# Optimization experiments

Measured on AMD Instinct MI355X. Metric: run time of the kernel, lower is better.

The kernel has to match this reference:

```python
import jax, jax.numpy as jnp
import numpy as np

N_POINTS = 1048576
N_LEVELS = 16
F = 2
BASE_RES = 16
FINEST_RES = 512
LOG2_HASH = 19
SIZES = [2 ** min(i + 1, LOG2_HASH) for i in range(N_LEVELS)]  # per-level table rows (powers of 2)
OFFS = np.concatenate([[0], np.cumsum(SIZES)]).astype(np.int64)  # static row offsets into packed table
TOTAL_ROWS = int(OFFS[-1])  # 131070
# hash primes from the torch module; uint32 wraparound matches int64 low-bit behavior
# because each table size is a power of two <= 2^19 < 2^32, so h % 2^k == low k bits.
P0, P1, P2, P3 = np.uint32(1), np.uint32(2654435761), np.uint32(29675113), np.uint32(123456789)
CORNERS = np.array([[0,0,0],[1,0,0],[0,1,0],[1,1,0],
                    [0,0,1],[1,0,1],[0,1,1],[1,1,1]], dtype=np.uint32)  # torch stacking order


def setup_inputs() -> dict:
    key = jax.random.key(0)
    k1, k2 = jax.random.split(key)
    coords = jax.random.uniform(k1, (N_POINTS, 3), dtype=jnp.float32, minval=-1.0, maxval=1.0)
    hash_init_scale = 0.001
    table = jax.random.uniform(k2, (TOTAL_ROWS, F), dtype=jnp.float32,
                               minval=-hash_init_scale, maxval=hash_init_scale)
    return {"coords": coords, "table": table}


def _encode(coords, table):
    corners = jnp.asarray(CORNERS)  # [8,3] uint32
    outs = []
    for level in range(N_LEVELS):
        res = min(BASE_RES * (2 ** level), FINEST_RES)
        cs = (coords + 1.0) * res           # [N,3]
        cf = jnp.floor(cs)
        frac = cs - cf                      # [N,3]
        base = cf.astype(jnp.uint32)        # coords >= -1 so floor >= 0
        c = base[None, :, :] + corners[:, None, :]   # [8,N,3]
        x, y, z = c[..., 0], c[..., 1], c[..., 2]
        h = x * P0
        h = h * P1 + y
        h = h * P2 + z
        h = h * P3
        h = (h & jnp.uint32(SIZES[level] - 1)).astype(jnp.int32)  # mod power-of-2 table size
        feats = table[int(OFFS[level]) + h]          # [8,N,F] gather
        tx = frac[..., 0:1]; ty = frac[..., 1:2]; tz = frac[..., 2:3]
        f = (feats[0] * (1 - tx) * (1 - ty) * (1 - tz)
             + feats[1] * tx * (1 - ty) * (1 - tz)
             + feats[2] * (1 - tx) * ty * (1 - tz)
             + feats[3] * tx * ty * (1 - tz)
             + feats[4] * (1 - tx) * (1 - ty) * tz
             + feats[5] * tx * (1 - ty) * tz
             + feats[6] * (1 - tx) * ty * tz
             + feats[7] * tx * ty * tz)              # [N,F]
        outs.append(f)
    return jnp.concatenate(outs, axis=-1)            # [N, N_LEVELS*F]


def reference(coords, table):
    return _encode(coords, table)
```

## Files before the change

### kernel.cpp

```cpp
#include <hip/hip_runtime.h>
#include <hip/hip_fp16.h>


#define BLOCK 1024
#define NBLOCKS 512
#define ITERS 16
#define STAGED_ROWS 32766
#define LDS_BYTES 131072

__device__ __forceinline__ float2 ldsRow(const unsigned* lds, unsigned idx) {
    unsigned u = lds[idx];
    __half2 h = *(__half2*)&u;
    return __half22float2(h);
}

#define PREP(FRES, HARR, WARR) \
    unsigned HARR[8]; float WARR[8]; { \
        const float csx = (px + 1.0f) * (FRES); \
        const float csy = (py + 1.0f) * (FRES); \
        const float csz = (pz + 1.0f) * (FRES); \
        const float cfx = floorf(csx), cfy = floorf(csy), cfz = floorf(csz); \
        const float tx = csx - cfx, ty = csy - cfy, tz = csz - cfz; \
        const unsigned hh = (unsigned)cfx * HA + (unsigned)cfy * HB + (unsigned)cfz * HC; \
        const float ux = 1.0f - tx, uy = 1.0f - ty, uz = 1.0f - tz; \
        WARR[0] = ux*uy*uz; WARR[1] = tx*uy*uz; WARR[2] = ux*ty*uz; WARR[3] = tx*ty*uz; \
        WARR[4] = ux*uy*tz; WARR[5] = tx*uy*tz; WARR[6] = ux*ty*tz; WARR[7] = tx*ty*tz; \
        HARR[0] = hh;           HARR[1] = hh + HA;           \
        HARR[2] = hh + HB;      HARR[3] = hh + HA + HB;      \
        HARR[4] = hh + HC;      HARR[5] = hh + HA + HC;      \
        HARR[6] = hh + HB + HC; HARR[7] = hh + HA + HB + HC; \
    }

#define GATHER_LDS(HARR, WARR, MASK, OFF, O0, O1) \
    { _Pragma("unroll") for (int c = 0; c < 8; ++c) { \
        float2 f = ldsRow(lds_tb, (OFF) + ((HARR[c]) & (MASK))); \
        (O0) += f.x * WARR[c]; (O1) += f.y * WARR[c]; } }

#define GATHER_GBL(HARR, WARR, MASK, OFF, O0, O1) \
    { _Pragma("unroll") for (int c = 0; c < 8; ++c) { \
        float2 f = tb[(OFF) + ((HARR[c]) & (MASK))]; \
        (O0) += f.x * WARR[c]; (O1) += f.y * WARR[c]; } }

__global__ __launch_bounds__(BLOCK) void ngp_encode_kernel(
    const float* __restrict__ coords,
    const float* __restrict__ table,
    float* __restrict__ out)
{
    extern __shared__ unsigned lds_tb[];

    {
        const float4* __restrict__ t4 = (const float4*)table;
        uint2* __restrict__ l2 = (uint2*)lds_tb;
        for (int r = threadIdx.x; r < STAGED_ROWS / 2; r += BLOCK) {
            float4 v = t4[r];
            __half2 a = __floats2half2_rn(v.x, v.y);
            __half2 b = __floats2half2_rn(v.z, v.w);
            uint2 u;
            u.x = *(unsigned*)&a;
            u.y = *(unsigned*)&b;
            l2[r] = u;
        }
    }
    __syncthreads();

    constexpr unsigned P1 = 2654435761u, P2 = 29675113u, P3 = 123456789u;
    constexpr unsigned HA = P1 * P2 * P3;
    constexpr unsigned HB = P2 * P3;
    constexpr unsigned HC = P3;

    const float2* __restrict__ tb = (const float2*)table;
    float4* __restrict__ out4 = (float4*)out;

    const int q = threadIdx.x & 7;
    const int l0 = 2 * q;
    const unsigned mask0 = (2u << l0) - 1u, off0 = mask0 - 1u;
    const unsigned mask1 = (4u << l0) - 1u, off1 = mask1 - 1u;
    const float fres0 = (l0 < 5) ? (float)(16 << l0) : 512.0f;
    const float fres1 = (l0 < 4) ? (float)(32 << l0) : 512.0f;

    for (int it = 0; it < ITERS; ++it) {
        const int t = (blockIdx.x * ITERS + it) * BLOCK + threadIdx.x;
        const int p = t >> 3;

        const float px = coords[3 * p + 0];
        const float py = coords[3 * p + 1];
        const float pz = coords[3 * p + 2];

        PREP(fres0, h0, w0)
        PREP(fres1, h1, w1)

        float o0 = 0.0f, o1 = 0.0f, o2 = 0.0f, o3 = 0.0f;
        if (q != 7) {
            GATHER_LDS(h0, w0, mask0, off0, o0, o1)
            GATHER_LDS(h1, w1, mask1, off1, o2, o3)
        } else {
            GATHER_GBL(h0, w0, mask0, off0, o0, o1)
            GATHER_GBL(h1, w1, mask1, off1, o2, o3)
        }

        out4[t] = make_float4(o0, o1, o2, o3);
    }
}

extern "C" void kernel_launch(void* const* d_in, const int* in_sizes, int n_in,
                              void* d_out, int out_size, void* d_ws, size_t ws_size,
                              hipStream_t stream) {
    const float* coords = (const float*)d_in[0];
    const float* table  = (const float*)d_in[1];
    float* out = (float*)d_out;

    hipFuncSetAttribute((const void*)ngp_encode_kernel,
                        hipFuncAttributeMaxDynamicSharedMemorySize,
                        LDS_BYTES);

    ngp_encode_kernel<<<NBLOCKS, BLOCK, LDS_BYTES, stream>>>(coords, table, out);
}
```

Measured before the change: 239.6 us.

## Remap work so each half-wave computes eight levels per point with LDS transpose

Replaces the 8-threads-per-point level split with two half-waves per 32 points: one half handles levels 0-7 from LDS, the other handles levels 8-15 with levels 13-15 from global memory. Finest-resolution hash/weight setup is computed once and shared across the high levels. Only the first 16382 rows are staged in LDS, freeing space for a swizzled per-wave transpose buffer used to produce coalesced float4 output stores. This removes redundant coordinate loads and PREP work and balances global gathers across lanes, at the cost of extra LDS traffic, register pressure, and a wave-local sync assumed via lgkmcnt wait.

```diff
diff --git a/kernel.cpp b/kernel.cpp
--- a/kernel.cpp
+++ b/kernel.cpp
@@ -4,14 +4,15 @@
 
 #define BLOCK 1024
 #define NBLOCKS 512
-#define ITERS 16
-#define STAGED_ROWS 32766
+#define ITERS 4
+#define STAGED_ROWS 16382
+#define TBL_LDS_BYTES 65536
 #define LDS_BYTES 131072
 
 __device__ __forceinline__ float2 ldsRow(const unsigned* lds, unsigned idx) {
     unsigned u = lds[idx];
-    __half2 h = *(__half2*)&u;
-    return __half22float2(h);
+    __half2 hh = *(__half2*)&u;
+    return __half22float2(hh);
 }
 
 #define PREP(FRES, HARR, WARR) \
@@ -31,22 +32,14 @@
         HARR[6] = hh + HB + HC; HARR[7] = hh + HA + HB + HC; \
     }
 
-#define GATHER_LDS(HARR, WARR, MASK, OFF, O0, O1) \
-    { _Pragma("unroll") for (int c = 0; c < 8; ++c) { \
-        float2 f = ldsRow(lds_tb, (OFF) + ((HARR[c]) & (MASK))); \
-        (O0) += f.x * WARR[c]; (O1) += f.y * WARR[c]; } }
-
-#define GATHER_GBL(HARR, WARR, MASK, OFF, O0, O1) \
-    { _Pragma("unroll") for (int c = 0; c < 8; ++c) { \
-        float2 f = tb[(OFF) + ((HARR[c]) & (MASK))]; \
-        (O0) += f.x * WARR[c]; (O1) += f.y * WARR[c]; } }
-
 __global__ __launch_bounds__(BLOCK) void ngp_encode_kernel(
     const float* __restrict__ coords,
     const float* __restrict__ table,
     float* __restrict__ out)
 {
-    extern __shared__ unsigned lds_tb[];
+    extern __shared__ unsigned char lds_raw[];
+    unsigned* lds_tb = (unsigned*)lds_raw;
+    float4* lds_tr   = (float4*)(lds_raw + TBL_LDS_BYTES);
 
     {
         const float4* __restrict__ t4 = (const float4*)table;
@@ -71,34 +64,86 @@
     const float2* __restrict__ tb = (const float2*)table;
     float4* __restrict__ out4 = (float4*)out;
 
-    const int q = threadIdx.x & 7;
-    const int l0 = 2 * q;
-    const unsigned mask0 = (2u << l0) - 1u, off0 = mask0 - 1u;
-    const unsigned mask1 = (4u << l0) - 1u, off1 = mask1 - 1u;
-    const float fres0 = (l0 < 5) ? (float)(16 << l0) : 512.0f;
-    const float fres1 = (l0 < 4) ? (float)(32 << l0) : 512.0f;
+    const int wv   = threadIdx.x >> 6;
+    const int lane = threadIdx.x & 63;
+    const int h    = lane >> 5;
+    const int pq   = lane & 31;
+    float4* trw = lds_tr + wv * 256;
 
     for (int it = 0; it < ITERS; ++it) {
-        const int t = (blockIdx.x * ITERS + it) * BLOCK + threadIdx.x;
-        const int p = t >> 3;
+        const int pb = blockIdx.x * 2048 + wv * 128 + it * 32;
+        const int p  = pb + pq;
 
         const float px = coords[3 * p + 0];
         const float py = coords[3 * p + 1];
         const float pz = coords[3 * p + 2];
 
-        PREP(fres0, h0, w0)
-        PREP(fres1, h1, w1)
+        PREP(512.0f, h5, w5)
 
-        float o0 = 0.0f, o1 = 0.0f, o2 = 0.0f, o3 = 0.0f;
-        if (q != 7) {
-            GATHER_LDS(h0, w0, mask0, off0, o0, o1)
-            GATHER_LDS(h1, w1, mask1, off1, o2, o3)
-        } else {
-            GATHER_GBL(h0, w0, mask0, off0, o0, o1)
-            GATHER_GBL(h1, w1, mask1, off1, o2, o3)
+        float acc[16];
+#pragma unroll
+        for (int i = 0; i < 16; ++i) acc[i] = 0.0f;
+
+#pragma unroll
+        for (int i = 0; i < 5; ++i) {
+            const float fres = (float)(16 << i);
+            PREP(fres, hs, ws)
+            const unsigned M0 = (2u << i) - 1u,       O0 = M0 - 1u;
+            const unsigned M1 = (2u << (i + 8)) - 1u, O1 = M1 - 1u;
+            const unsigned msk = h ? M1 : M0;
+            const unsigned off = h ? O1 : O0;
+#pragma unroll
+            for (int c = 0; c < 8; ++c) {
+                const unsigned hc = h ? h5[c] : hs[c];
+                const float    wc = h ? w5[c] : ws[c];
+                float2 f = ldsRow(lds_tb, off + (hc & msk));
+                acc[2 * i + 0] += f.x * wc;
+                acc[2 * i + 1] += f.y * wc;
+            }
         }
 
-        out4[t] = make_float4(o0, o1, o2, o3);
+#pragma unroll
+        for (int i = 5; i < 8; ++i) {
+            const unsigned M0 = (2u << i) - 1u,       O0 = M0 - 1u;
+            const unsigned M1 = (2u << (i + 8)) - 1u, O1 = M1 - 1u;
+            float2 g[8];
+            if (h) {
+#pragma unroll
+                for (int c = 0; c < 8; ++c)
+                    g[c] = tb[O1 + (h5[c] & M1)];
+            }
+            if (!h) {
+#pragma unroll
+                for (int c = 0; c < 8; ++c) {
+                    float2 f = ldsRow(lds_tb, O0 + (h5[c] & M0));
+                    acc[2 * i + 0] += f.x * w5[c];
+                    acc[2 * i + 1] += f.y * w5[c];
+                }
+            }
+            if (h) {
+#pragma unroll
+                for (int c = 0; c < 8; ++c) {
+                    acc[2 * i + 0] += g[c].x * w5[c];
+                    acc[2 * i + 1] += g[c].y * w5[c];
+                }
+            }
+        }
+
+#pragma unroll
+        for (int j = 0; j < 4; ++j) {
+            const int s = (h * 4 + j) ^ (pq & 7);
+            trw[pq * 8 + s] =
+                make_float4(acc[4 * j + 0], acc[4 * j + 1],
+                            acc[4 * j + 2], acc[4 * j + 3]);
+        }
+        asm volatile("s_waitcnt lgkmcnt(0)" ::: "memory");
+#pragma unroll
+        for (int k = 0; k < 4; ++k) {
+            const int m  = k * 64 + lane;
+            const int pm = m >> 3, qm = m & 7;
+            float4 v = trw[pm * 8 + (qm ^ (pm & 7))];
+            out4[(size_t)pb * 8 + m] = v;
+        }
     }
 }
 
```

Measured after the change: 241.5 us. No clear change (+0.8%).
